# Performance work log

Hardware: AMD Instinct MI355X
Metric: run time of the kernel (lower is better)

The kernel has to match this reference:

```python
import jax, jax.numpy as jnp
import numpy as np

T, B, I, H, R, O = 128, 32, 128, 128, 100, 64


def setup_inputs() -> dict:
    key = jax.random.key(0)
    ks = jax.random.split(key, 8)
    # xavier-ish / kaiming-ish scales so tanh doesn't saturate
    return {
        "x": jax.random.normal(ks[0], (T, B, I), jnp.float32),
        "C": jax.random.uniform(ks[1], (R, R), jnp.float32) / R,
        "W_ih": jax.random.normal(ks[2], (R, I, H), jnp.float32) * (1.0 / np.sqrt(I)),
        "W_hh": jax.random.normal(ks[3], (R, H, H), jnp.float32) * (1.0 / np.sqrt(H)),
        "W_rhh": jax.random.normal(ks[4], (R, H, H), jnp.float32) * (1.0 / np.sqrt(H)),
        "bias": jax.random.normal(ks[5], (R, H), jnp.float32) * 0.1,
        "W_out": jax.random.normal(ks[6], (R * H, O), jnp.float32) * (1.0 / np.sqrt(R * H)),
        "b_out": jax.random.normal(ks[7], (O,), jnp.float32) * 0.1,
    }


def reference(x, C, W_ih, W_hh, W_rhh, bias, b_out, W_out):
    seq_len, bs, _ = x.shape
    num_regions, hidden = bias.shape
    H0 = jnp.zeros((num_regions, bs, hidden), dtype=x.dtype)

    def step(Hprev, x_t):
        # input drive: per-region projection of the shared input
        inp = jnp.einsum('bi,rih->rbh', x_t, W_ih)
        # local recurrence
        loc = jnp.einsum('rbh,rhg->rbg', Hprev, W_hh)
        # connectome-weighted message sum: recurrent_sum[j] = sum_i C[i,j] * Hprev[i]
        msg = jnp.einsum('ij,ibh->jbh', C, Hprev)
        cross = jnp.einsum('rbh,rhg->rbg', msg, W_rhh)
        Ht = jnp.tanh(inp + loc + cross + bias[:, None, :])
        return Ht, Ht

    _, H_hist = jax.lax.scan(step, H0, x)          # [T, R, B, H]
    H_hist = H_hist.transpose(0, 2, 1, 3).reshape(seq_len, bs, num_regions * hidden)
    return H_hist @ W_out + b_out                   # [T, B, O]
```

## Files before the change

### kernel.cpp

```cpp
#include <hip/hip_runtime.h>
#include <hip/hip_bf16.h>

typedef unsigned char u8;
typedef unsigned short u16;
typedef __attribute__((ext_vector_type(8))) short bf16x8;
typedef __attribute__((ext_vector_type(8))) _Float16 f16x8;
typedef __attribute__((ext_vector_type(4))) float f32x4;
typedef __attribute__((ext_vector_type(2))) float f32x2;
typedef __attribute__((ext_vector_type(4))) int i32x4;

#define T_ 128
#define B_ 32
#define I_ 128
#define H_ 128
#define R_ 100
#define O_ 64
#define NWG2 200
#define NRED 4
#define SLICE (R_*B_*H_)
#define ROWB  (B_*H_)
#define XOFF  (T_*B_*I_)
#define WOFF  (R_*H_*H_)
#define OOFF  (O_*R_*H_)
#define PB    (16*O_)
#define SFBASE 6400
#define XCNTOFF 7168

__device__ __forceinline__ float b2f(u16 u) {
  unsigned x = ((unsigned)u) << 16; float f; __builtin_memcpy(&f, &x, 4); return f;
}
__device__ __forceinline__ u16 f2b(float f) {
  unsigned x; __builtin_memcpy(&x, &f, 4);
  unsigned lsb = (x >> 16) & 1u;
  x += 0x7fffu + lsb;
  return (u16)(x >> 16);
}
__device__ __forceinline__ void split2(float f, u16& hi, u16& lo) {
  hi = f2b(f);
  lo = f2b(f - b2f(hi));
}
__device__ __forceinline__ u16 f2h(float f) {
  _Float16 h = (_Float16)f; u16 u; __builtin_memcpy(&u, &h, 2); return u;
}
__device__ __forceinline__ float h2f(u16 u) {
  _Float16 h; __builtin_memcpy(&h, &u, 2); return (float)h;
}
__device__ __forceinline__ void split2h(float f, u16& hi, u16& lo) {
  _Float16 h = (_Float16)f;
  _Float16 l = (_Float16)(f - (float)h);
  __builtin_memcpy(&hi, &h, 2); __builtin_memcpy(&lo, &l, 2);
}
__device__ __forceinline__ float fast_tanh(float v) {
  float a = fabsf(v);
  float e = __expf(-2.f * a);
  float th = (1.f - e) * __builtin_amdgcn_rcpf(1.f + e);
  return v < 0.f ? -th : th;
}

#if __has_builtin(__builtin_amdgcn_cvt_pk_f32_fp8) && __has_builtin(__builtin_amdgcn_cvt_pk_fp8_f32)
#define HW_FP8 1
#endif

__device__ __forceinline__ unsigned enc1_fp8(float f) {
  unsigned x; __builtin_memcpy(&x, &f, 4);
  unsigned s = (x >> 31) << 7;
  float a = fabsf(f);
  if (!(a < 464.f)) return s | 0x7E;
  if (a == 0.f) return s;
  int E = (int)((x >> 23) & 0xFF) - 127;
  if (E < -6) E = -6;
  float sc; unsigned sb = (unsigned)(127 + 3 - E) << 23; __builtin_memcpy(&sc, &sb, 4);
  int q = (int)rintf(a * sc);
  if (q == 16) { E += 1; q = 8; }
  if (E > 8) return s | 0x7E;
  unsigned ee, mm;
  if (q < 8) { ee = 0; mm = (unsigned)q; }
  else { ee = (unsigned)(E + 7); mm = (unsigned)(q - 8); }
  return s | (ee << 3) | mm;
}
__device__ __forceinline__ float dec1_fp8(unsigned b) {
  unsigned s = (b >> 7) & 1, ee = (b >> 3) & 0xF, mm = b & 7;
  float v;
  if (ee == 0) v = (float)mm * 0.001953125f;
  else { unsigned fb = ((ee + 120) << 23) | (mm << 20); __builtin_memcpy(&v, &fb, 4); }
  return s ? -v : v;
}
__device__ __forceinline__ void fp8x4_to_2x2(unsigned u, f32x2& a, f32x2& b) {
#ifdef HW_FP8
  a = __builtin_amdgcn_cvt_pk_f32_fp8((int)u, false);
  b = __builtin_amdgcn_cvt_pk_f32_fp8((int)u, true);
#else
  a[0] = dec1_fp8(u & 255); a[1] = dec1_fp8((u >> 8) & 255);
  b[0] = dec1_fp8((u >> 16) & 255); b[1] = dec1_fp8(u >> 24);
#endif
}
__device__ __forceinline__ unsigned f32x4_to_fp8(float f0, float f1, float f2, float f3) {
#ifdef HW_FP8
  int v = __builtin_amdgcn_cvt_pk_fp8_f32(f0, f1, 0, false);
  v = __builtin_amdgcn_cvt_pk_fp8_f32(f2, f3, v, true);
  return (unsigned)v;
#else
  return enc1_fp8(f0) | (enc1_fp8(f1) << 8) | (enc1_fp8(f2) << 16) | (enc1_fp8(f3) << 24);
#endif
}
__device__ __forceinline__ i32x4 pack16(const u16* p) {
  i32x4 o;
  #pragma unroll
  for (int g = 0; g < 4; ++g)
    o[g] = (int)f32x4_to_fp8(h2f(p[g*4+0]), h2f(p[g*4+1]), h2f(p[g*4+2]), h2f(p[g*4+3]));
  return o;
}

__device__ __forceinline__ f32x2 pk_fma(f32x2 a, f32x2 b, f32x2 c) {
  f32x2 d;
  asm("v_pk_fma_f32 %0, %1, %2, %3" : "=v"(d) : "v"(a), "v"(b), "v"(c));
  return d;
}

__device__ __forceinline__ void st16_sc(void* p, i32x4 v) {
  asm volatile("global_store_dwordx4 %0, %1, off sc1" :: "v"(p), "v"(v) : "memory");
}
__device__ __forceinline__ void ld4_issue0(int& r, const void* p) {
  asm volatile("global_load_dword %0, %1, off sc0" : "=v"(r) : "v"(p));
}
__device__ __forceinline__ void wait_vm() { asm volatile("s_waitcnt vmcnt(0)" ::: "memory"); }
#define WAITV(N) do { asm volatile("s_waitcnt vmcnt(" #N ")" ::: "memory"); \
                      __builtin_amdgcn_sched_barrier(0); } while (0)

__device__ __forceinline__ float aldf(const float* p) {
  return __hip_atomic_load((float*)p, __ATOMIC_RELAXED, __HIP_MEMORY_SCOPE_AGENT);
}
__device__ __forceinline__ void astf(float* p, float v) {
  __hip_atomic_store(p, v, __ATOMIC_RELAXED, __HIP_MEMORY_SCOPE_AGENT);
}

__global__ void __launch_bounds__(256)
probe_dtype(const u16* __restrict__ x, int* __restrict__ mode)
{
  __shared__ int cnt;
  if (threadIdx.x == 0) cnt = 0;
  __syncthreads();
  int bad = 0;
  for (int i = threadIdx.x; i < 8192; i += 256) {
    int ex = (x[i] >> 7) & 0xFF;
    if (ex >= 134) ++bad;
  }
  atomicAdd(&cnt, bad);
  __syncthreads();
  if (threadIdx.x == 0) *mode = (cnt > 256) ? 1 : 0;
}

__device__ __forceinline__ float load_in(const void* p, size_t i, int f32) {
  return f32 ? ((const float*)p)[i] : b2f(((const u16*)p)[i]);
}

__global__ void __launch_bounds__(256)
conv_split(const void* __restrict__ src, u16* __restrict__ hi, u16* __restrict__ lo,
           const int* __restrict__ mode, int n)
{
  int i = blockIdx.x * 256 + threadIdx.x;
  if (i < n) { u16 h, l; split2(load_in(src, i, *mode), h, l); hi[i] = h; lo[i] = l; }
}

__global__ void __launch_bounds__(256)
conv_vec(const void* __restrict__ src, float* __restrict__ dst,
         const int* __restrict__ mode, int n)
{
  int i = blockIdx.x * 256 + threadIdx.x;
  if (i < n) dst[i] = load_in(src, i, *mode);
}

__global__ void __launch_bounds__(256)
transpose_kn2(const void* __restrict__ in, u16* __restrict__ ohi, u16* __restrict__ olo,
              int KK, int NN, const int* __restrict__ mode, int fmt)
{
  __shared__ float tile[32][33];
  const int f32 = *mode;
  int ntk = KK >> 5, ntn = NN >> 5;
  int bid = blockIdx.x;
  int m  = bid / (ntk * ntn);
  int rem = bid % (ntk * ntn);
  int kt = rem / ntn, nt = rem % ntn;
  size_t base = (size_t)m * KK * NN;
  int tid = threadIdx.x;
  int tc = tid & 31, tr0 = tid >> 5;
  #pragma unroll
  for (int rr = 0; rr < 4; ++rr) {
    int tr = tr0 + rr * 8;
    tile[tr][tc] = load_in(in, base + (size_t)(kt*32 + tr) * NN + nt*32 + tc, f32);
  }
  __syncthreads();
  #pragma unroll
  for (int rr = 0; rr < 4; ++rr) {
    int tr = tr0 + rr * 8;
    u16 h, l;
    if (fmt) split2h(tile[tc][tr], h, l); else split2(tile[tc][tr], h, l);
    size_t di = base + (size_t)(nt*32 + tr) * KK + kt*32 + tc;
    ohi[di] = h; olo[di] = l;
  }
}

__device__ __forceinline__ void wait_flags(const int* f, int cnt, int target, int tid) {
  if (tid < cnt) {
    int sp = 0;
    while (__hip_atomic_load((int*)&f[tid * 32], __ATOMIC_RELAXED, __HIP_MEMORY_SCOPE_AGENT) < target) {
      __builtin_amdgcn_s_sleep(2);
      if (++sp > (1 << 18)) break;
    }
  }
  asm volatile("" ::: "memory");
  __syncthreads();
}
__device__ __forceinline__ void poll1(const int* f, int target) {
  int sp = 0;
  while (__hip_atomic_load((int*)f, __ATOMIC_RELAXED, __HIP_MEMORY_SCOPE_AGENT) < target) {
    if (++sp > 48) __builtin_amdgcn_s_sleep(2);
    if (sp > (1 << 20)) break;
  }
  asm volatile("" ::: "memory");
}
__device__ __forceinline__ void post_flag(int* f, int v) {
  __hip_atomic_store(f, v, __ATOMIC_RELAXED, __HIP_MEMORY_SCOPE_AGENT);
}

__device__ __forceinline__ f32x4 mfma_(bf16x8 a, bf16x8 b, f32x4 c) {
  return __builtin_amdgcn_mfma_f32_16x16x32_bf16(a, b, c, 0, 0, 0);
}
__device__ __forceinline__ f32x4 mfma_h(f16x8 a, f16x8 b, f32x4 c) {
  return __builtin_amdgcn_mfma_f32_16x16x32_f16(a, b, c, 0, 0, 0);
}

#define MIXROW(Q, CI) do { \
  f32x2 c2_ = csh2[(CI)]; \
  f32x2 a_, b_; fp8x4_to_2x2((unsigned)(Q), a_, b_); \
  macc01 = pk_fma(a_, c2_, macc01); \
  macc23 = pk_fma(b_, c2_, macc23); \
} while (0)

#define ISSUE8(Q, P) do { _Pragma("unroll") \
  for (int k_ = 0; k_ < 8; ++k_) ld4_issue0(Q[k_], (P) + (size_t)k_ * ROWB); } while (0)
#define ISSUE4(Q, P) do { _Pragma("unroll") \
  for (int k_ = 0; k_ < 4; ++k_) ld4_issue0(Q[k_], (P) + (size_t)k_ * ROWB); } while (0)
#define PROC8(Q, CI) do { _Pragma("unroll") \
  for (int k_ = 0; k_ < 8; ++k_) MIXROW(Q[k_], (CI) + k_); } while (0)
#define PROC4(Q, CI) do { _Pragma("unroll") \
  for (int k_ = 0; k_ < 4; ++k_) MIXROW(Q[k_], (CI) + k_); } while (0)

__global__ void __launch_bounds__(512, 2)
rnn_kernel(const u16* __restrict__ x,
           u8* __restrict__ Hb,
           const u16* __restrict__ WihT, const u16* __restrict__ WhhT,
           const u16* __restrict__ WrhhT,
           const float* __restrict__ Cf,
           const float* __restrict__ biasf,
           const u16* __restrict__ WoutT,
           float* __restrict__ part,
           u16* __restrict__ part2,
           const float* __restrict__ boutf,
           float* __restrict__ out, int* __restrict__ flags, int bigpart)
{
  const int w    = blockIdx.x;
  const int tid  = threadIdx.x;
  const int lane = tid & 63;
  const int wv   = tid >> 6;
  const int l15  = lane & 15;
  const int quad = lane >> 4;

  __shared__ __align__(16) u16 Hmhi[16 * 136];
  __shared__ __align__(16) u16 Hmlo[16 * 136];
  __shared__ __align__(16) u16 msgS[16 * 136];
  __shared__ __align__(16) u16 mS[16 * 128];
  __shared__ __align__(16) f32x2 csh2[112];
  __shared__ int shRank;

  if (w >= NWG2) {
    const int aw = w - NWG2;
    for (int t = 0; t < T_; ++t) {
      wait_flags(flags + 1, NWG2, t + 1, tid);
      const float* pb = part + (size_t)(t & 1) * (NWG2 * PB);
      int e = aw * 512 + tid;
      int b = e >> 6, o = e & 63;
      int ue = b >> 4, bl = b & 15;
      float s = 0.f;
      #pragma unroll 4
      for (int r2 = 0; r2 < R_; ++r2)
        s += aldf(pb + (size_t)(r2 * 2 + ue) * PB + bl * O_ + o);
      out[(size_t)t * (B_*O_) + e] = s + boutf[o];
    }
    return;
  }

  int xcd;
  asm volatile("s_getreg_b32 %0, hwreg(HW_REG_XCC_ID)" : "=s"(xcd));
  xcd &= 7;
  if (tid == 0)
    shRank = __hip_atomic_fetch_add(&flags[XCNTOFF + xcd], 1,
                                    __ATOMIC_RELAXED, __HIP_MEMORY_SCOPE_AGENT);

  const int r = w >> 1;
  const int u = w & 1;
  const int col = wv * 16 + l15;
  int* invf = &flags[SFBASE + xcd * 32];

  for (int e = tid; e < 16 * 136; e += 512) { Hmhi[e] = 0; Hmlo[e] = 0; }
  if (tid < R_) {
    float c = Cf[(size_t)tid * R_ + r];
    f32x2 c2; c2[0] = c; c2[1] = c;
    csh2[tid] = c2;
  }
  __syncthreads();
  const int rank = shRank;

  bf16x8 w0h[4], w0l[4], w1h[4], w1l[4];
  f16x8  w2h[4], w2l[4];
  bf16x8 boh[4], bol[4];
  {
    const u16* B0 = WihT  + (size_t)r * (H_*I_) + (size_t)col * 128;
    const u16* B1 = WhhT  + (size_t)r * (H_*H_) + (size_t)col * 128;
    const u16* B2 = WrhhT + (size_t)r * (H_*H_) + (size_t)col * 128;
    const int o = (wv >= 4) ? ((wv - 4) * 16 + l15) : l15;
    const u16* Bo = WoutT + (size_t)o * (R_*H_) + (size_t)r * H_;
    #pragma unroll
    for (int kk = 0; kk < 4; ++kk) {
      int koff = kk * 32 + quad * 8;
      w0h[kk] = *(const bf16x8*)(B0 + koff);
      w0l[kk] = *(const bf16x8*)(B0 + WOFF + koff);
      w1h[kk] = *(const bf16x8*)(B1 + koff);
      w1l[kk] = *(const bf16x8*)(B1 + WOFF + koff);
      w2h[kk] = *(const f16x8*)(B2 + koff);
      w2l[kk] = *(const f16x8*)(B2 + WOFF + koff);
      boh[kk] = *(const bf16x8*)(Bo + koff);
      bol[kk] = *(const bf16x8*)(Bo + OOFF + koff);
    }
  }
  const float bs = biasf[r*H_ + col];

  for (int t = 0; t < T_; ++t) {
    f32x4 accX = {0,0,0,0}, accH = {0,0,0,0};
    {
      const u16* Ax = x + (size_t)t * (B_*I_) + (size_t)(u*16) * I_;
      #pragma unroll
      for (int kk = 0; kk < 4; ++kk) {
        int koff = kk * 32 + quad * 8;
        const u16* pa = Ax + (size_t)l15 * 128 + koff;
        bf16x8 ah = *(const bf16x8*)pa, al = *(const bf16x8*)(pa + XOFF);
        accX = mfma_(al, w0h[kk], mfma_(ah, w0l[kk], mfma_(ah, w0h[kk], accX)));
        bf16x8 hh = *(const bf16x8*)(&Hmhi[l15 * 136 + koff]);
        bf16x8 hl = *(const bf16x8*)(&Hmlo[l15 * 136 + koff]);
        accH = mfma_(hl, w1h[kk], mfma_(hh, w1l[kk], mfma_(hh, w1h[kk], accH)));
      }
    }

    if (t > 0) {
      const int par = (t + 1) & 1;

      if (tid < R_) poll1(&flags[((tid << 1) | u) * 32], t);
      else if (tid == 128) poll1(invf, t);
      __syncthreads();

      const u8* Hs = Hb + (size_t)par * SLICE
                   + (size_t)(u*16 + (tid >> 5)) * H_ + (tid & 31) * 4;
      f32x2 macc01 = {0.f, 0.f}, macc23 = {0.f, 0.f};
      int bufA[8], bufB[8], bufC[8];
      const u8* pI = Hs;
      ISSUE8(bufA, pI); pI += (size_t)8 * ROWB;
      ISSUE8(bufB, pI); pI += (size_t)8 * ROWB;
      ISSUE8(bufC, pI); pI += (size_t)8 * ROWB;
      int ci = 0;
      for (int it = 0; it < 3; ++it) {
        WAITV(16); PROC8(bufA, ci); ci += 8; ISSUE8(bufA, pI); pI += (size_t)8 * ROWB;
        WAITV(16); PROC8(bufB, ci); ci += 8; ISSUE8(bufB, pI); pI += (size_t)8 * ROWB;
        WAITV(16); PROC8(bufC, ci); ci += 8; ISSUE8(bufC, pI); pI += (size_t)8 * ROWB;
      }
      WAITV(16); PROC8(bufA, 72); ISSUE4(bufA, pI);
      WAITV(12); PROC8(bufB, 80);
      WAITV(4);  PROC8(bufC, 88);
      WAITV(0);  PROC4(bufA, 96);

      union { u16 h[4]; unsigned long long v; } mw;
      mw.h[0]=f2h(macc01[0]); mw.h[1]=f2h(macc01[1]);
      mw.h[2]=f2h(macc23[0]); mw.h[3]=f2h(macc23[1]);
      *(unsigned long long*)&msgS[(tid >> 5) * 136 + (tid & 31) * 4] = mw.v;
      __syncthreads();

      #pragma unroll
      for (int kk = 0; kk < 4; ++kk) {
        int koff = kk * 32 + quad * 8;
        f16x8 a0 = *(const f16x8*)(&msgS[l15 * 136 + koff]);
        accX = mfma_h(a0, w2l[kk], mfma_h(a0, w2h[kk], accX));
      }
    } else {
      __syncthreads();
    }

    {
      #pragma unroll
      for (int rr = 0; rr < 4; ++rr) {
        int br = quad*4 + rr;
        u16 h, l;
        float v = fast_tanh(accX[rr] + accH[rr] + bs);
        split2(v, h, l);
        Hmhi[br*136 + col] = h; Hmlo[br*136 + col] = l;
        mS[br*128 + col] = f2h(v);
      }
    }
    __syncthreads();

    if (tid < 64) {
      int row = tid >> 2, c = (tid & 3) * 32;
      u8* Hn = Hb + (size_t)(t & 1) * SLICE + (size_t)r * ROWB
             + (size_t)(u*16 + row) * H_ + c;
      const u16* p = &mS[row * 128 + c];
      st16_sc(Hn,      pack16(p));
      st16_sc(Hn + 16, pack16(p + 16));
      wait_vm();
      if (tid == 0) post_flag(&flags[w * 32 + 0], t + 1);
    }

    if (rank == 0) {
      if (tid < NWG2) poll1(&flags[tid * 32], t);
      __syncthreads();
      if (tid == 0) {
        __builtin_amdgcn_fence(__ATOMIC_ACQUIRE, "agent");
        wait_vm();
        post_flag(invf, t + 1);
      }
    }

    {
      if (wv >= 4) {
        const int o = (wv - 4) * 16 + l15;
        f32x4 y0 = {0,0,0,0};
        #pragma unroll
        for (int kk = 0; kk < 4; ++kk) {
          int koff = kk * 32 + quad * 8;
          bf16x8 ah = *(const bf16x8*)(&Hmhi[l15 * 136 + koff]);
          bf16x8 al = *(const bf16x8*)(&Hmlo[l15 * 136 + koff]);
          y0 = mfma_(al, boh[kk], mfma_(ah, bol[kk], mfma_(ah, boh[kk], y0)));
        }
        if (bigpart) {
          u16* pp = part2 + ((size_t)t * R_ + r) * (B_*O_);
          #pragma unroll
          for (int rr = 0; rr < 4; ++rr)
            pp[(u*16 + quad*4 + rr)*O_ + o] = f2b(y0[rr]);
        } else {
          float* pp = part + (size_t)(t & 1) * (NWG2 * PB) + (size_t)w * PB;
          #pragma unroll
          for (int rr = 0; rr < 4; ++rr)
            astf(pp + (quad*4 + rr)*O_ + o, y0[rr]);
        }
      }
      if (!bigpart) {
        __syncthreads();
        if (tid == 0) post_flag(&flags[w * 32 + 1], t + 1);
      }
    }
  }
}

__global__ void __launch_bounds__(256)
reduce_out(const u16* __restrict__ part2, const float* __restrict__ boutf,
           float* __restrict__ out)
{
  const int t = blockIdx.x, tid = threadIdx.x;
  const u16* base = part2 + (size_t)t * R_ * (B_*O_) + tid * 8;
  float acc[8] = {0,0,0,0,0,0,0,0};
  for (int r2 = 0; r2 < R_; ++r2) {
    bf16x8 v = *(const bf16x8*)(base + (size_t)r2 * (B_*O_));
    #pragma unroll
    for (int j = 0; j < 8; ++j) acc[j] += b2f((u16)v[j]);
  }
  int e = tid * 8;
  #pragma unroll
  for (int j = 0; j < 8; ++j)
    out[(size_t)t * (B_*O_) + e + j] = acc[j] + boutf[(e + j) & (O_-1)];
}

extern "C" void kernel_launch(void* const* d_in, const int* in_sizes, int n_in,
                              void* d_out, int out_size, void* d_ws, size_t ws_size,
                              hipStream_t stream) {
  const void* xp    = d_in[0];
  const void* Cp    = d_in[1];
  const void* Wih   = d_in[2];
  const void* Whh   = d_in[3];
  const void* Wrhh  = d_in[4];
  const void* biasp = d_in[5];
  const void* Wout  = d_in[6];
  const void* boutp = d_in[7];
  float* outp = (float*)d_out;

  char* ws = (char*)d_ws;
  size_t off = 0;
  auto carve = [&](size_t bytes) -> void* {
    void* p = ws + off;
    off += (bytes + 255) & ~(size_t)255;
    return p;
  };
  u16*   xb    = (u16*)carve((size_t)2 * XOFF * 2);
  u8*    Hb    = (u8*)carve((size_t)2 * SLICE);
  u16*   wihT  = (u16*)carve((size_t)2 * WOFF * 2);
  u16*   whhT  = (u16*)carve((size_t)2 * WOFF * 2);
  u16*   wrhhT = (u16*)carve((size_t)2 * WOFF * 2);
  u16*   woutT = (u16*)carve((size_t)2 * OOFF * 2);
  float* cfp   = (float*)carve((size_t)R_ * R_ * 4);
  float* biasf = (float*)carve((size_t)R_ * H_ * 4);
  float* boutf = (float*)carve((size_t)O_ * 4);
  float* partp = (float*)carve((size_t)2 * NWG2 * PB * 4);
  int*   flagp = (int*)carve((size_t)256 * 32 * 4);
  int*   modep = (int*)carve(256);
  size_t part2_bytes = (size_t)T_ * R_ * B_ * O_ * 2;
  u16*   part2 = (u16*)(ws + off);
  int bigpart = (off + part2_bytes) <= ws_size;

  hipMemsetAsync(flagp, 0, (size_t)256 * 32 * 4, stream);

  probe_dtype<<<dim3(1), dim3(256), 0, stream>>>((const u16*)xp, modep);
  conv_split<<<dim3((XOFF + 255)/256), dim3(256), 0, stream>>>(xp, xb, xb + XOFF, modep, XOFF);
  conv_vec<<<dim3((R_*H_ + 255)/256), dim3(256), 0, stream>>>(biasp, biasf, modep, R_*H_);
  conv_vec<<<dim3(1), dim3(256), 0, stream>>>(boutp, boutf, modep, O_);
  conv_vec<<<dim3((R_*R_ + 255)/256), dim3(256), 0, stream>>>(Cp, cfp, modep, R_*R_);

  transpose_kn2<<<dim3(R_ * 16), dim3(256), 0, stream>>>(Wih,  wihT,  wihT  + WOFF, I_, H_, modep, 0);
  transpose_kn2<<<dim3(R_ * 16), dim3(256), 0, stream>>>(Whh,  whhT,  whhT  + WOFF, H_, H_, modep, 0);
  transpose_kn2<<<dim3(R_ * 16), dim3(256), 0, stream>>>(Wrhh, wrhhT, wrhhT + WOFF, H_, H_, modep, 1);
  transpose_kn2<<<dim3(800),     dim3(256), 0, stream>>>(Wout, woutT, woutT + OOFF, R_ * H_, O_, modep, 0);

  int nblk = bigpart ? NWG2 : (NWG2 + NRED);
  rnn_kernel<<<dim3(nblk), dim3(512), 0, stream>>>(
      xb, Hb, wihT, whhT, wrhhT, cfp, biasf, woutT,
      partp, part2, boutf, outp, flagp, bigpart);

  if (bigpart)
    reduce_out<<<dim3(T_), dim3(256), 0, stream>>>(part2, boutf, outp);
}
```

Before: 992.1 us.

## Warp-specialize RNN step: producer waves store/poll while consumer waves gate-stream connectome mix

Splits the 512-thread workgroup into roles. Waves 0-3 do the input/local MFMAs and stream the cross-region message mix, gated per 8-region group by LDS ready flags. Waves 4-7 publish the previous step's FP8 hidden state, poll the global flags into those LDS ready counters, and run the delayed output projection. Hidden-state and staging buffers become double-buffered so the store of step t-1 and the output projection overlap with step t. The mix loads widen to dwordx2 with half as many threads per row, and the launch bound drops the min-2-blocks hint. The aim is to start consuming remote hidden states as soon as each region arrives instead of waiting behind a full barrier. In exchange, synchronization is more intricate and the finer-grained spinning may add latency.

```diff
diff --git a/kernel.cpp b/kernel.cpp
--- a/kernel.cpp
+++ b/kernel.cpp
@@ -8,6 +8,7 @@
 typedef __attribute__((ext_vector_type(4))) float f32x4;
 typedef __attribute__((ext_vector_type(2))) float f32x2;
 typedef __attribute__((ext_vector_type(4))) int i32x4;
+typedef __attribute__((ext_vector_type(2))) int i32x2;
 
 #define T_ 128
 #define B_ 32
@@ -120,8 +121,8 @@
 __device__ __forceinline__ void st16_sc(void* p, i32x4 v) {
   asm volatile("global_store_dwordx4 %0, %1, off sc1" :: "v"(p), "v"(v) : "memory");
 }
-__device__ __forceinline__ void ld4_issue0(int& r, const void* p) {
-  asm volatile("global_load_dword %0, %1, off sc0" : "=v"(r) : "v"(p));
+__device__ __forceinline__ void ld8_issue0(i32x2& r, const void* p) {
+  asm volatile("global_load_dwordx2 %0, %1, off sc0" : "=v"(r) : "v"(p));
 }
 __device__ __forceinline__ void wait_vm() { asm volatile("s_waitcnt vmcnt(0)" ::: "memory"); }
 #define WAITV(N) do { asm volatile("s_waitcnt vmcnt(" #N ")" ::: "memory"); \
@@ -132,6 +133,12 @@
 }
 __device__ __forceinline__ void astf(float* p, float v) {
   __hip_atomic_store(p, v, __ATOMIC_RELAXED, __HIP_MEMORY_SCOPE_AGENT);
+}
+__device__ __forceinline__ int ldsrdy(const int* p) {
+  return __hip_atomic_load((int*)p, __ATOMIC_RELAXED, __HIP_MEMORY_SCOPE_WORKGROUP);
+}
+__device__ __forceinline__ void ldswr(int* p, int v) {
+  __hip_atomic_store(p, v, __ATOMIC_RELAXED, __HIP_MEMORY_SCOPE_WORKGROUP);
 }
 
 __global__ void __launch_bounds__(256)
@@ -230,23 +237,42 @@
   return __builtin_amdgcn_mfma_f32_16x16x32_f16(a, b, c, 0, 0, 0);
 }
 
-#define MIXROW(Q, CI) do { \
+#define MIXROW8(Q, CI) do { \
   f32x2 c2_ = csh2[(CI)]; \
-  f32x2 a_, b_; fp8x4_to_2x2((unsigned)(Q), a_, b_); \
-  macc01 = pk_fma(a_, c2_, macc01); \
-  macc23 = pk_fma(b_, c2_, macc23); \
+  f32x2 a0_, a1_, b0_, b1_; \
+  fp8x4_to_2x2((unsigned)(Q)[0], a0_, a1_); \
+  fp8x4_to_2x2((unsigned)(Q)[1], b0_, b1_); \
+  macc0 = pk_fma(a0_, c2_, macc0); macc1 = pk_fma(a1_, c2_, macc1); \
+  macc2 = pk_fma(b0_, c2_, macc2); macc3 = pk_fma(b1_, c2_, macc3); \
 } while (0)
 
-#define ISSUE8(Q, P) do { _Pragma("unroll") \
-  for (int k_ = 0; k_ < 8; ++k_) ld4_issue0(Q[k_], (P) + (size_t)k_ * ROWB); } while (0)
-#define ISSUE4(Q, P) do { _Pragma("unroll") \
-  for (int k_ = 0; k_ < 4; ++k_) ld4_issue0(Q[k_], (P) + (size_t)k_ * ROWB); } while (0)
-#define PROC8(Q, CI) do { _Pragma("unroll") \
-  for (int k_ = 0; k_ < 8; ++k_) MIXROW(Q[k_], (CI) + k_); } while (0)
-#define PROC4(Q, CI) do { _Pragma("unroll") \
-  for (int k_ = 0; k_ < 4; ++k_) MIXROW(Q[k_], (CI) + k_); } while (0)
-
-__global__ void __launch_bounds__(512, 2)
+#define ISSUE8M(Q, G) do { _Pragma("unroll") \
+  for (int k_ = 0; k_ < 8; ++k_) ld8_issue0(Q[k_], Hs + (size_t)((G)*8 + k_) * ROWB); } while (0)
+#define ISSUE4M(Q, G) do { _Pragma("unroll") \
+  for (int k_ = 0; k_ < 4; ++k_) ld8_issue0(Q[k_], Hs + (size_t)((G)*8 + k_) * ROWB); } while (0)
+#define PROC8M(Q, G) do { _Pragma("unroll") \
+  for (int k_ = 0; k_ < 8; ++k_) MIXROW8(Q[k_], (G)*8 + k_); } while (0)
+#define PROC4M(Q, G) do { _Pragma("unroll") \
+  for (int k_ = 0; k_ < 4; ++k_) MIXROW8(Q[k_], (G)*8 + k_); } while (0)
+
+#define GATE(G) do { \
+  int gsp_ = 0; \
+  for (;;) { \
+    int mn_ = 0x7fffffff; \
+    _Pragma("unroll") \
+    for (int j_ = 0; j_ < 8; ++j_) { \
+      int id_ = (G)*8 + j_; if (id_ > 99) id_ = 99; \
+      int v_ = ldsrdy(&readyS[id_]); mn_ = v_ < mn_ ? v_ : mn_; \
+    } \
+    if ((G) == 0) { int v_ = ldsrdy(&readyS[100]); mn_ = v_ < mn_ ? v_ : mn_; } \
+    if (mn_ >= t) break; \
+    __builtin_amdgcn_s_sleep(1); \
+    if (++gsp_ > (1 << 20)) break; \
+  } \
+  asm volatile("" ::: "memory"); \
+} while (0)
+
+__global__ void __launch_bounds__(512)
 rnn_kernel(const u16* __restrict__ x,
            u8* __restrict__ Hb,
            const u16* __restrict__ WihT, const u16* __restrict__ WhhT,
@@ -266,11 +292,13 @@
   const int l15  = lane & 15;
   const int quad = lane >> 4;
 
-  __shared__ __align__(16) u16 Hmhi[16 * 136];
-  __shared__ __align__(16) u16 Hmlo[16 * 136];
-  __shared__ __align__(16) u16 msgS[16 * 136];
-  __shared__ __align__(16) u16 mS[16 * 128];
+  __shared__ __align__(16) u16 Hmhi[2 * 2176];
+  __shared__ __align__(16) u16 Hmlo[2 * 2176];
+  __shared__ __align__(16) u16 msgS[2176];
+  __shared__ __align__(16) u16 mS2[2 * 2048];
   __shared__ __align__(16) f32x2 csh2[112];
+  __shared__ int readyS[104];
+  __shared__ int pcnt;
   __shared__ int shRank;
 
   if (w >= NWG2) {
@@ -302,7 +330,9 @@
   const int col = wv * 16 + l15;
   int* invf = &flags[SFBASE + xcd * 32];
 
-  for (int e = tid; e < 16 * 136; e += 512) { Hmhi[e] = 0; Hmlo[e] = 0; }
+  for (int e = tid; e < 2 * 2176; e += 512) { Hmhi[e] = 0; Hmlo[e] = 0; }
+  if (tid < 104) readyS[tid] = 0;
+  if (tid == 0) pcnt = 0;
   if (tid < R_) {
     float c = Cf[(size_t)tid * R_ + r];
     f32x2 c2; c2[0] = c; c2[1] = c;
@@ -335,126 +365,175 @@
   }
   const float bs = biasf[r*H_ + col];
 
+  auto do_outproj = [&](int pt) {
+    const int o = (wv - 4) * 16 + l15;
+    const u16* Hh = &Hmhi[(pt & 1) * 2176];
+    const u16* Hl = &Hmlo[(pt & 1) * 2176];
+    f32x4 y0 = {0,0,0,0};
+    #pragma unroll
+    for (int kk = 0; kk < 4; ++kk) {
+      int koff = kk * 32 + quad * 8;
+      bf16x8 ah = *(const bf16x8*)(&Hh[l15 * 136 + koff]);
+      bf16x8 al = *(const bf16x8*)(&Hl[l15 * 136 + koff]);
+      y0 = mfma_(al, boh[kk], mfma_(ah, bol[kk], mfma_(ah, boh[kk], y0)));
+    }
+    if (bigpart) {
+      u16* pp = part2 + ((size_t)pt * R_ + r) * (B_*O_);
+      #pragma unroll
+      for (int rr = 0; rr < 4; ++rr)
+        pp[(u*16 + quad*4 + rr)*O_ + o] = f2b(y0[rr]);
+    } else {
+      float* pp = part + (size_t)(pt & 1) * (NWG2 * PB) + (size_t)w * PB;
+      #pragma unroll
+      for (int rr = 0; rr < 4; ++rr)
+        astf(pp + (quad*4 + rr)*O_ + o, y0[rr]);
+    }
+  };
+
   for (int t = 0; t < T_; ++t) {
     f32x4 accX = {0,0,0,0}, accH = {0,0,0,0};
-    {
+
+    auto do_seg01 = [&]() {
       const u16* Ax = x + (size_t)t * (B_*I_) + (size_t)(u*16) * I_;
+      const u16* Hh = &Hmhi[((t + 1) & 1) * 2176];
+      const u16* Hl = &Hmlo[((t + 1) & 1) * 2176];
       #pragma unroll
       for (int kk = 0; kk < 4; ++kk) {
         int koff = kk * 32 + quad * 8;
         const u16* pa = Ax + (size_t)l15 * 128 + koff;
         bf16x8 ah = *(const bf16x8*)pa, al = *(const bf16x8*)(pa + XOFF);
         accX = mfma_(al, w0h[kk], mfma_(ah, w0l[kk], mfma_(ah, w0h[kk], accX)));
-        bf16x8 hh = *(const bf16x8*)(&Hmhi[l15 * 136 + koff]);
-        bf16x8 hl = *(const bf16x8*)(&Hmlo[l15 * 136 + koff]);
+        bf16x8 hh = *(const bf16x8*)(&Hh[l15 * 136 + koff]);
+        bf16x8 hl = *(const bf16x8*)(&Hl[l15 * 136 + koff]);
         accH = mfma_(hl, w1h[kk], mfma_(hh, w1l[kk], mfma_(hh, w1h[kk], accH)));
       }
-    }
+    };
+
+    if (wv < 4) {
+      do_seg01();
+      if (t > 0) {
+        const int par = (t + 1) & 1;
+        const int b  = tid >> 4;
+        const int h0 = (tid & 15) * 8;
+        const u8* Hs = Hb + (size_t)par * SLICE
+                     + (size_t)(u*16 + b) * H_ + h0;
+        f32x2 macc0={0,0}, macc1={0,0}, macc2={0,0}, macc3={0,0};
+        i32x2 bufA[8], bufB[8], bufC[8];
+        wait_vm();
+        GATE(0);  ISSUE8M(bufA, 0);
+        GATE(1);  ISSUE8M(bufB, 1);
+        GATE(2);  ISSUE8M(bufC, 2);
+        WAITV(16); PROC8M(bufA, 0);  GATE(3);  ISSUE8M(bufA, 3);
+        WAITV(16); PROC8M(bufB, 1);  GATE(4);  ISSUE8M(bufB, 4);
+        WAITV(16); PROC8M(bufC, 2);  GATE(5);  ISSUE8M(bufC, 5);
+        WAITV(16); PROC8M(bufA, 3);  GATE(6);  ISSUE8M(bufA, 6);
+        WAITV(16); PROC8M(bufB, 4);  GATE(7);  ISSUE8M(bufB, 7);
+        WAITV(16); PROC8M(bufC, 5);  GATE(8);  ISSUE8M(bufC, 8);
+        WAITV(16); PROC8M(bufA, 6);  GATE(9);  ISSUE8M(bufA, 9);
+        WAITV(16); PROC8M(bufB, 7);  GATE(10); ISSUE8M(bufB, 10);
+        WAITV(16); PROC8M(bufC, 8);  GATE(11); ISSUE8M(bufC, 11);
+        WAITV(16); PROC8M(bufA, 9);  GATE(12); ISSUE4M(bufA, 12);
+        WAITV(12); PROC8M(bufB, 10);
+        WAITV(4);  PROC8M(bufC, 11);
+        WAITV(0);  PROC4M(bufA, 12);
+
+        union { u16 h[8]; i32x4 v; } mw;
+        mw.h[0]=f2h(macc0[0]); mw.h[1]=f2h(macc0[1]);
+        mw.h[2]=f2h(macc1[0]); mw.h[3]=f2h(macc1[1]);
+        mw.h[4]=f2h(macc2[0]); mw.h[5]=f2h(macc2[1]);
+        mw.h[6]=f2h(macc3[0]); mw.h[7]=f2h(macc3[1]);
+        *(i32x4*)&msgS[b * 136 + h0] = mw.v;
+      }
+    } else {
+      const int stid = tid - 256;
+      if (t > 0) {
+        if (stid < 64) {
+          int row = stid >> 2, c = (stid & 3) * 32;
+          u8* Hn = Hb + (size_t)((t - 1) & 1) * SLICE + (size_t)r * ROWB
+                 + (size_t)(u*16 + row) * H_ + c;
+          const u16* p = &mS2[((t - 1) & 1) * 2048 + row * 128 + c];
+          st16_sc(Hn,      pack16(p));
+          st16_sc(Hn + 16, pack16(p + 16));
+          wait_vm();
+          if (stid == 0) post_flag(&flags[w * 32], t);
+        }
+        if (rank == 0) {
+          if (stid < NWG2) {
+            poll1(&flags[stid * 32], t);
+            if ((stid & 1) == u) ldswr(&readyS[stid >> 1], t);
+            __hip_atomic_fetch_add(&pcnt, 1, __ATOMIC_RELAXED,
+                                   __HIP_MEMORY_SCOPE_WORKGROUP);
+          } else if (stid == 200) {
+            poll1(invf, t);
+            ldswr(&readyS[100], t);
+          }
+          if (stid == 0) {
+            int sp = 0;
+            while (__hip_atomic_load(&pcnt, __ATOMIC_RELAXED,
+                                     __HIP_MEMORY_SCOPE_WORKGROUP) < NWG2 * t) {
+              __builtin_amdgcn_s_sleep(2);
+              if (++sp > (1 << 20)) break;
+            }
+            __builtin_amdgcn_fence(__ATOMIC_ACQUIRE, "agent");
+            wait_vm();
+            post_flag(invf, t + 1);
+          }
+        } else {
+          if (stid >= 64 && stid < 164) {
+            int i = stid - 64;
+            poll1(&flags[((i << 1) | u) * 32], t);
+            ldswr(&readyS[i], t);
+          } else if (stid == 164) {
+            poll1(invf, t);
+            ldswr(&readyS[100], t);
+          }
+        }
+        do_outproj(t - 1);
+      } else {
+        if (rank == 0 && stid == 0) {
+          __builtin_amdgcn_fence(__ATOMIC_ACQUIRE, "agent");
+          wait_vm();
+          post_flag(invf, 1);
+        }
+      }
+      do_seg01();
+    }
+
+    __syncthreads();
+
+    if (!bigpart && t > 0 && tid == 256)
+      post_flag(&flags[w * 32 + 1], t);
 
     if (t > 0) {
-      const int par = (t + 1) & 1;
-
-      if (tid < R_) poll1(&flags[((tid << 1) | u) * 32], t);
-      else if (tid == 128) poll1(invf, t);
-      __syncthreads();
-
-      const u8* Hs = Hb + (size_t)par * SLICE
-                   + (size_t)(u*16 + (tid >> 5)) * H_ + (tid & 31) * 4;
-      f32x2 macc01 = {0.f, 0.f}, macc23 = {0.f, 0.f};
-      int bufA[8], bufB[8], bufC[8];
-      const u8* pI = Hs;
-      ISSUE8(bufA, pI); pI += (size_t)8 * ROWB;
-      ISSUE8(bufB, pI); pI += (size_t)8 * ROWB;
-      ISSUE8(bufC, pI); pI += (size_t)8 * ROWB;
-      int ci = 0;
-      for (int it = 0; it < 3; ++it) {
-        WAITV(16); PROC8(bufA, ci); ci += 8; ISSUE8(bufA, pI); pI += (size_t)8 * ROWB;
-        WAITV(16); PROC8(bufB, ci); ci += 8; ISSUE8(bufB, pI); pI += (size_t)8 * ROWB;
-        WAITV(16); PROC8(bufC, ci); ci += 8; ISSUE8(bufC, pI); pI += (size_t)8 * ROWB;
-      }
-      WAITV(16); PROC8(bufA, 72); ISSUE4(bufA, pI);
-      WAITV(12); PROC8(bufB, 80);
-      WAITV(4);  PROC8(bufC, 88);
-      WAITV(0);  PROC4(bufA, 96);
-
-      union { u16 h[4]; unsigned long long v; } mw;
-      mw.h[0]=f2h(macc01[0]); mw.h[1]=f2h(macc01[1]);
-      mw.h[2]=f2h(macc23[0]); mw.h[3]=f2h(macc23[1]);
-      *(unsigned long long*)&msgS[(tid >> 5) * 136 + (tid & 31) * 4] = mw.v;
-      __syncthreads();
-
       #pragma unroll
       for (int kk = 0; kk < 4; ++kk) {
         int koff = kk * 32 + quad * 8;
         f16x8 a0 = *(const f16x8*)(&msgS[l15 * 136 + koff]);
         accX = mfma_h(a0, w2l[kk], mfma_h(a0, w2h[kk], accX));
       }
-    } else {
-      __syncthreads();
     }
 
     {
+      u16* Hh = &Hmhi[(t & 1) * 2176];
+      u16* Hl = &Hmlo[(t & 1) * 2176];
+      u16* mSc = &mS2[(t & 1) * 2048];
       #pragma unroll
       for (int rr = 0; rr < 4; ++rr) {
         int br = quad*4 + rr;
         u16 h, l;
         float v = fast_tanh(accX[rr] + accH[rr] + bs);
         split2(v, h, l);
-        Hmhi[br*136 + col] = h; Hmlo[br*136 + col] = l;
-        mS[br*128 + col] = f2h(v);
+        Hh[br*136 + col] = h; Hl[br*136 + col] = l;
+        mSc[br*128 + col] = f2h(v);
       }
     }
     __syncthreads();
-
-    if (tid < 64) {
-      int row = tid >> 2, c = (tid & 3) * 32;
-      u8* Hn = Hb + (size_t)(t & 1) * SLICE + (size_t)r * ROWB
-             + (size_t)(u*16 + row) * H_ + c;
-      const u16* p = &mS[row * 128 + c];
-      st16_sc(Hn,      pack16(p));
-      st16_sc(Hn + 16, pack16(p + 16));
-      wait_vm();
-      if (tid == 0) post_flag(&flags[w * 32 + 0], t + 1);
-    }
-
-    if (rank == 0) {
-      if (tid < NWG2) poll1(&flags[tid * 32], t);
-      __syncthreads();
-      if (tid == 0) {
-        __builtin_amdgcn_fence(__ATOMIC_ACQUIRE, "agent");
-        wait_vm();
-        post_flag(invf, t + 1);
-      }
-    }
-
-    {
-      if (wv >= 4) {
-        const int o = (wv - 4) * 16 + l15;
-        f32x4 y0 = {0,0,0,0};
-        #pragma unroll
-        for (int kk = 0; kk < 4; ++kk) {
-          int koff = kk * 32 + quad * 8;
-          bf16x8 ah = *(const bf16x8*)(&Hmhi[l15 * 136 + koff]);
-          bf16x8 al = *(const bf16x8*)(&Hmlo[l15 * 136 + koff]);
-          y0 = mfma_(al, boh[kk], mfma_(ah, bol[kk], mfma_(ah, boh[kk], y0)));
-        }
-        if (bigpart) {
-          u16* pp = part2 + ((size_t)t * R_ + r) * (B_*O_);
-          #pragma unroll
-          for (int rr = 0; rr < 4; ++rr)
-            pp[(u*16 + quad*4 + rr)*O_ + o] = f2b(y0[rr]);
-        } else {
-          float* pp = part + (size_t)(t & 1) * (NWG2 * PB) + (size_t)w * PB;
-          #pragma unroll
-          for (int rr = 0; rr < 4; ++rr)
-            astf(pp + (quad*4 + rr)*O_ + o, y0[rr]);
-        }
-      }
-      if (!bigpart) {
-        __syncthreads();
-        if (tid == 0) post_flag(&flags[w * 32 + 1], t + 1);
-      }
-    }
+  }
+
+  if (wv >= 4) do_outproj(T_ - 1);
+  if (!bigpart) {
+    __syncthreads();
+    if (tid == 256) post_flag(&flags[w * 32 + 1], T_);
   }
 }
 
```

Measured after the change: 1.069 ms. 1.08x slower.

## Merge batch-half workgroups so each region workgroup processes both chains

Applied to the files above, without the earlier changes.

The persistent RNN kernel drops from 200 workgroups (one per region and batch half) to 100, each handling one region and running both 16-row batch chains back to back every timestep. Shared-memory state is doubled so each chain keeps its own copy, and the output projection moves into each chain's slot. The aim is to cut cross-workgroup flag polling and synchronisation and to let one chain's compute overlap the other's wait. The cost is that each workgroup now does twice the serial work per step on the recurrence-critical path, and only half as many compute units are used.

```diff
diff --git a/kernel.cpp b/kernel.cpp
--- a/kernel.cpp
+++ b/kernel.cpp
@@ -15,6 +15,7 @@
 #define H_ 128
 #define R_ 100
 #define O_ 64
+#define NWGW 100
 #define NWG2 200
 #define NRED 4
 #define SLICE (R_*B_*H_)
@@ -266,17 +267,17 @@
   const int l15  = lane & 15;
   const int quad = lane >> 4;
 
-  __shared__ __align__(16) u16 Hmhi[16 * 136];
-  __shared__ __align__(16) u16 Hmlo[16 * 136];
-  __shared__ __align__(16) u16 msgS[16 * 136];
-  __shared__ __align__(16) u16 mS[16 * 128];
+  __shared__ __align__(16) u16 Hmhi[2 * 2176];
+  __shared__ __align__(16) u16 Hmlo[2 * 2176];
+  __shared__ __align__(16) u16 msgS[2176];
+  __shared__ __align__(16) u16 mS[2 * 2048];
   __shared__ __align__(16) f32x2 csh2[112];
   __shared__ int shRank;
 
-  if (w >= NWG2) {
-    const int aw = w - NWG2;
+  if (w >= NWGW) {
+    const int aw = w - NWGW;
     for (int t = 0; t < T_; ++t) {
-      wait_flags(flags + 1, NWG2, t + 1, tid);
+      wait_flags(flags + 1, NWGW, t + 1, tid);
       const float* pb = part + (size_t)(t & 1) * (NWG2 * PB);
       int e = aw * 512 + tid;
       int b = e >> 6, o = e & 63;
@@ -297,12 +298,11 @@
     shRank = __hip_atomic_fetch_add(&flags[XCNTOFF + xcd], 1,
                                     __ATOMIC_RELAXED, __HIP_MEMORY_SCOPE_AGENT);
 
-  const int r = w >> 1;
-  const int u = w & 1;
+  const int r = w;
   const int col = wv * 16 + l15;
   int* invf = &flags[SFBASE + xcd * 32];
 
-  for (int e = tid; e < 16 * 136; e += 512) { Hmhi[e] = 0; Hmlo[e] = 0; }
+  for (int e = tid; e < 2 * 2176; e += 512) { Hmhi[e] = 0; Hmlo[e] = 0; }
   if (tid < R_) {
     float c = Cf[(size_t)tid * R_ + r];
     f32x2 c2; c2[0] = c; c2[1] = c;
@@ -335,31 +335,32 @@
   }
   const float bs = biasf[r*H_ + col];
 
-  for (int t = 0; t < T_; ++t) {
+  auto slot = [&](int t, int chain) {
     f32x4 accX = {0,0,0,0}, accH = {0,0,0,0};
+    u16* Hh = Hmhi + chain * 2176;
+    u16* Hl = Hmlo + chain * 2176;
     {
-      const u16* Ax = x + (size_t)t * (B_*I_) + (size_t)(u*16) * I_;
+      const u16* Ax = x + (size_t)t * (B_*I_) + (size_t)(chain*16) * I_;
       #pragma unroll
       for (int kk = 0; kk < 4; ++kk) {
         int koff = kk * 32 + quad * 8;
         const u16* pa = Ax + (size_t)l15 * 128 + koff;
         bf16x8 ah = *(const bf16x8*)pa, al = *(const bf16x8*)(pa + XOFF);
         accX = mfma_(al, w0h[kk], mfma_(ah, w0l[kk], mfma_(ah, w0h[kk], accX)));
-        bf16x8 hh = *(const bf16x8*)(&Hmhi[l15 * 136 + koff]);
-        bf16x8 hl = *(const bf16x8*)(&Hmlo[l15 * 136 + koff]);
+        bf16x8 hh = *(const bf16x8*)(&Hh[l15 * 136 + koff]);
+        bf16x8 hl = *(const bf16x8*)(&Hl[l15 * 136 + koff]);
         accH = mfma_(hl, w1h[kk], mfma_(hh, w1l[kk], mfma_(hh, w1h[kk], accH)));
       }
     }
 
     if (t > 0) {
+      if (tid < R_) poll1(&flags[((tid << 1) | chain) * 32], t);
+      else if (chain == 0 && tid == 128) poll1(invf, t);
+      __syncthreads();
+
       const int par = (t + 1) & 1;
-
-      if (tid < R_) poll1(&flags[((tid << 1) | u) * 32], t);
-      else if (tid == 128) poll1(invf, t);
-      __syncthreads();
-
       const u8* Hs = Hb + (size_t)par * SLICE
-                   + (size_t)(u*16 + (tid >> 5)) * H_ + (tid & 31) * 4;
+                   + (size_t)(chain*16 + (tid >> 5)) * H_ + (tid & 31) * 4;
       f32x2 macc01 = {0.f, 0.f}, macc23 = {0.f, 0.f};
       int bufA[8], bufB[8], bufC[8];
       const u8* pI = Hs;
@@ -394,14 +395,15 @@
     }
 
     {
+      u16* mSc = mS + chain * 2048;
       #pragma unroll
       for (int rr = 0; rr < 4; ++rr) {
         int br = quad*4 + rr;
         u16 h, l;
         float v = fast_tanh(accX[rr] + accH[rr] + bs);
         split2(v, h, l);
-        Hmhi[br*136 + col] = h; Hmlo[br*136 + col] = l;
-        mS[br*128 + col] = f2h(v);
+        Hh[br*136 + col] = h; Hl[br*136 + col] = l;
+        mSc[br*128 + col] = f2h(v);
       }
     }
     __syncthreads();
@@ -409,13 +411,41 @@
     if (tid < 64) {
       int row = tid >> 2, c = (tid & 3) * 32;
       u8* Hn = Hb + (size_t)(t & 1) * SLICE + (size_t)r * ROWB
-             + (size_t)(u*16 + row) * H_ + c;
-      const u16* p = &mS[row * 128 + c];
+             + (size_t)(chain*16 + row) * H_ + c;
+      const u16* p = &mS[chain * 2048 + row * 128 + c];
       st16_sc(Hn,      pack16(p));
       st16_sc(Hn + 16, pack16(p + 16));
       wait_vm();
-      if (tid == 0) post_flag(&flags[w * 32 + 0], t + 1);
-    }
+      if (tid == 0) post_flag(&flags[(r * 2 + chain) * 32], t + 1);
+    }
+
+    if (wv >= 4) {
+      const int o = (wv - 4) * 16 + l15;
+      f32x4 y0 = {0,0,0,0};
+      #pragma unroll
+      for (int kk = 0; kk < 4; ++kk) {
+        int koff = kk * 32 + quad * 8;
+        bf16x8 ah = *(const bf16x8*)(&Hh[l15 * 136 + koff]);
+        bf16x8 al = *(const bf16x8*)(&Hl[l15 * 136 + koff]);
+        y0 = mfma_(al, boh[kk], mfma_(ah, bol[kk], mfma_(ah, boh[kk], y0)));
+      }
+      if (bigpart) {
+        u16* pp = part2 + ((size_t)t * R_ + r) * (B_*O_);
+        #pragma unroll
+        for (int rr = 0; rr < 4; ++rr)
+          pp[(chain*16 + quad*4 + rr)*O_ + o] = f2b(y0[rr]);
+      } else {
+        float* pp = part + (size_t)(t & 1) * (NWG2 * PB)
+                  + (size_t)(r * 2 + chain) * PB;
+        #pragma unroll
+        for (int rr = 0; rr < 4; ++rr)
+          astf(pp + (quad*4 + rr)*O_ + o, y0[rr]);
+      }
+    }
+  };
+
+  for (int t = 0; t < T_; ++t) {
+    slot(t, 0);
 
     if (rank == 0) {
       if (tid < NWG2) poll1(&flags[tid * 32], t);
@@ -427,33 +457,11 @@
       }
     }
 
-    {
-      if (wv >= 4) {
-        const int o = (wv - 4) * 16 + l15;
-        f32x4 y0 = {0,0,0,0};
-        #pragma unroll
-        for (int kk = 0; kk < 4; ++kk) {
-          int koff = kk * 32 + quad * 8;
-          bf16x8 ah = *(const bf16x8*)(&Hmhi[l15 * 136 + koff]);
-          bf16x8 al = *(const bf16x8*)(&Hmlo[l15 * 136 + koff]);
-          y0 = mfma_(al, boh[kk], mfma_(ah, bol[kk], mfma_(ah, boh[kk], y0)));
-        }
-        if (bigpart) {
-          u16* pp = part2 + ((size_t)t * R_ + r) * (B_*O_);
-          #pragma unroll
-          for (int rr = 0; rr < 4; ++rr)
-            pp[(u*16 + quad*4 + rr)*O_ + o] = f2b(y0[rr]);
-        } else {
-          float* pp = part + (size_t)(t & 1) * (NWG2 * PB) + (size_t)w * PB;
-          #pragma unroll
-          for (int rr = 0; rr < 4; ++rr)
-            astf(pp + (quad*4 + rr)*O_ + o, y0[rr]);
-        }
-      }
-      if (!bigpart) {
-        __syncthreads();
-        if (tid == 0) post_flag(&flags[w * 32 + 1], t + 1);
-      }
+    slot(t, 1);
+
+    if (!bigpart) {
+      __syncthreads();
+      if (tid == 0) post_flag(&flags[w * 32 + 1], t + 1);
     }
   }
 }
@@ -525,7 +533,7 @@
   transpose_kn2<<<dim3(R_ * 16), dim3(256), 0, stream>>>(Wrhh, wrhhT, wrhhT + WOFF, H_, H_, modep, 1);
   transpose_kn2<<<dim3(800),     dim3(256), 0, stream>>>(Wout, woutT, woutT + OOFF, R_ * H_, O_, modep, 0);
 
-  int nblk = bigpart ? NWG2 : (NWG2 + NRED);
+  int nblk = bigpart ? NWGW : (NWGW + NRED);
   rnn_kernel<<<dim3(nblk), dim3(512), 0, stream>>>(
       xb, Hb, wihT, whhT, wrhhT, cfp, biasf, woutT,
       partp, part2, boutf, outp, flagp, bigpart);
```

Result: slower. 1.789 ms (+80.4%).

## Overlap input/local MFMAs with message loads and encode fp8 before staging

Applied to the files above, without the earlier changes.

The x-operand loads are hoisted to the top of each step. The input and local-recurrence MFMA segment is moved so it runs after the first cross-region H slices have been issued, letting the MFMAs hide the global load latency of the connectome message gather. The fp8 encoding of the new hidden state now happens per thread right after tanh, and the result is staged in LDS as bytes. This lets the store warps write packed fp8 directly instead of converting 32 values each. The extra wait_vm and the held x registers add register pressure and may reorder memory waits.

```diff
diff --git a/kernel.cpp b/kernel.cpp
--- a/kernel.cpp
+++ b/kernel.cpp
@@ -102,13 +102,6 @@
 #else
   return enc1_fp8(f0) | (enc1_fp8(f1) << 8) | (enc1_fp8(f2) << 16) | (enc1_fp8(f3) << 24);
 #endif
-}
-__device__ __forceinline__ i32x4 pack16(const u16* p) {
-  i32x4 o;
-  #pragma unroll
-  for (int g = 0; g < 4; ++g)
-    o[g] = (int)f32x4_to_fp8(h2f(p[g*4+0]), h2f(p[g*4+1]), h2f(p[g*4+2]), h2f(p[g*4+3]));
-  return o;
 }
 
 __device__ __forceinline__ f32x2 pk_fma(f32x2 a, f32x2 b, f32x2 c) {
@@ -269,7 +262,7 @@
   __shared__ __align__(16) u16 Hmhi[16 * 136];
   __shared__ __align__(16) u16 Hmlo[16 * 136];
   __shared__ __align__(16) u16 msgS[16 * 136];
-  __shared__ __align__(16) u16 mS[16 * 128];
+  __shared__ __align__(16) u8  mS8[16 * 128];
   __shared__ __align__(16) f32x2 csh2[112];
   __shared__ int shRank;
 
@@ -337,19 +330,29 @@
 
   for (int t = 0; t < T_; ++t) {
     f32x4 accX = {0,0,0,0}, accH = {0,0,0,0};
+
+    bf16x8 xah[4], xal[4];
     {
       const u16* Ax = x + (size_t)t * (B_*I_) + (size_t)(u*16) * I_;
       #pragma unroll
       for (int kk = 0; kk < 4; ++kk) {
+        const u16* pa = Ax + (size_t)l15 * 128 + kk * 32 + quad * 8;
+        xah[kk] = *(const bf16x8*)pa;
+        xal[kk] = *(const bf16x8*)(pa + XOFF);
+      }
+    }
+
+    auto seg01 = [&]() {
+      #pragma unroll
+      for (int kk = 0; kk < 4; ++kk) {
         int koff = kk * 32 + quad * 8;
-        const u16* pa = Ax + (size_t)l15 * 128 + koff;
-        bf16x8 ah = *(const bf16x8*)pa, al = *(const bf16x8*)(pa + XOFF);
-        accX = mfma_(al, w0h[kk], mfma_(ah, w0l[kk], mfma_(ah, w0h[kk], accX)));
+        accX = mfma_(xal[kk], w0h[kk],
+               mfma_(xah[kk], w0l[kk], mfma_(xah[kk], w0h[kk], accX)));
         bf16x8 hh = *(const bf16x8*)(&Hmhi[l15 * 136 + koff]);
         bf16x8 hl = *(const bf16x8*)(&Hmlo[l15 * 136 + koff]);
         accH = mfma_(hl, w1h[kk], mfma_(hh, w1l[kk], mfma_(hh, w1h[kk], accH)));
       }
-    }
+    };
 
     if (t > 0) {
       const int par = (t + 1) & 1;
@@ -357,6 +360,7 @@
       if (tid < R_) poll1(&flags[((tid << 1) | u) * 32], t);
       else if (tid == 128) poll1(invf, t);
       __syncthreads();
+      wait_vm();
 
       const u8* Hs = Hb + (size_t)par * SLICE
                    + (size_t)(u*16 + (tid >> 5)) * H_ + (tid & 31) * 4;
@@ -366,6 +370,9 @@
       ISSUE8(bufA, pI); pI += (size_t)8 * ROWB;
       ISSUE8(bufB, pI); pI += (size_t)8 * ROWB;
       ISSUE8(bufC, pI); pI += (size_t)8 * ROWB;
+
+      seg01();
+
       int ci = 0;
       for (int it = 0; it < 3; ++it) {
         WAITV(16); PROC8(bufA, ci); ci += 8; ISSUE8(bufA, pI); pI += (size_t)8 * ROWB;
@@ -390,19 +397,25 @@
         accX = mfma_h(a0, w2l[kk], mfma_h(a0, w2h[kk], accX));
       }
     } else {
+      seg01();
       __syncthreads();
     }
 
     {
+      float vv[4];
       #pragma unroll
       for (int rr = 0; rr < 4; ++rr) {
-        int br = quad*4 + rr;
         u16 h, l;
         float v = fast_tanh(accX[rr] + accH[rr] + bs);
         split2(v, h, l);
+        int br = quad*4 + rr;
         Hmhi[br*136 + col] = h; Hmlo[br*136 + col] = l;
-        mS[br*128 + col] = f2h(v);
-      }
+        vv[rr] = h2f(f2h(v));
+      }
+      unsigned pk = f32x4_to_fp8(vv[0], vv[1], vv[2], vv[3]);
+      #pragma unroll
+      for (int rr = 0; rr < 4; ++rr)
+        mS8[(quad*4 + rr)*128 + col] = (u8)(pk >> (8*rr));
     }
     __syncthreads();
 
@@ -410,9 +423,9 @@
       int row = tid >> 2, c = (tid & 3) * 32;
       u8* Hn = Hb + (size_t)(t & 1) * SLICE + (size_t)r * ROWB
              + (size_t)(u*16 + row) * H_ + c;
-      const u16* p = &mS[row * 128 + c];
-      st16_sc(Hn,      pack16(p));
-      st16_sc(Hn + 16, pack16(p + 16));
+      const u8* p = &mS8[row * 128 + c];
+      st16_sc(Hn,      *(const i32x4*)p);
+      st16_sc(Hn + 16, *(const i32x4*)(p + 16));
       wait_vm();
       if (tid == 0) post_flag(&flags[w * 32 + 0], t + 1);
     }
```

After: 1.009 ms. About the same (+1.7%).
